# Performance work log

Measured on AMD Instinct MI355X. Metric: run time of the kernel, lower is better.

Reference implementation:

```python
import jax, jax.numpy as jnp
import numpy as np

BITS = 4
MAXQ = (1 << BITS) - 1          # 15
PACK = 32 // BITS               # 8 values per int32
IN_F = 4096
OUT_F = 11008


def setup_inputs() -> dict:
    key = jax.random.key(0)
    k1, k2, k3, k4, k5 = jax.random.split(key, 5)
    x = jax.random.normal(k1, (8, IN_F), dtype=jnp.float32)
    qweight = jax.random.randint(k2, (IN_F // 32 * BITS, OUT_F), 0, 2147483647, dtype=jnp.int32)
    qzeros = jax.random.randint(k3, (1, OUT_F // 32 * BITS), 0, 2147483647, dtype=jnp.int32)
    scales = jax.random.uniform(k4, (1, OUT_F), dtype=jnp.float32, minval=1e-3, maxval=2e-2)
    bias = jax.random.normal(k5, (OUT_F,), dtype=jnp.float32)
    return {"x": x, "qweight": qweight, "qzeros": qzeros, "scales": scales, "bias": bias}


def reference(x, qweight, qzeros, scales, bias):
    # GPTQ-style unpack: each int32 packs PACK values of BITS bits, LSB first.
    shifts = jnp.arange(0, 32, BITS, dtype=jnp.int32)  # wf
    # unpack weights: (IN_F//PACK, OUT_F) -> (IN_F//PACK, PACK, OUT_F) -> (IN_F, OUT_F)
    w = (qweight[:, None, :] >> shifts[None, :, None]) & MAXQ
    w = w.reshape(IN_F, OUT_F).astype(scales.dtype)
    # unpack zeros: (1, OUT_F//PACK) -> (1, OUT_F//PACK, PACK) -> (1, OUT_F), +1 per GPTQ convention
    z = ((qzeros[:, :, None] >> shifts[None, None, :]) & MAXQ) + 1
    z = z.reshape(1, OUT_F).astype(scales.dtype)
    # single quantization group (group_size == infeatures, g_idx all zeros)
    W = scales * (w - z)                      # (IN_F, OUT_F)
    return x @ W + bias
```

## Files before the change

kernel.cpp:

```cpp
#include <hip/hip_runtime.h>

#define IN_F 4096
#define OUT_F 11008
#define M 8
#define KROWS 512
#define KSLICES 16
#define ROWS_PER_SLICE (KROWS / KSLICES)

__global__ __launch_bounds__(256) void init_out_kernel(
    const float* __restrict__ bias, float* __restrict__ out)
{
    int idx = blockIdx.x * 256 + threadIdx.x;
    if (idx < M * OUT_F) {
        out[idx] = bias[idx % OUT_F];
    }
}

__global__ __launch_bounds__(256) void gptq_gemm_kernel(
    const float* __restrict__ x,
    const int*   __restrict__ qw,
    const int*   __restrict__ qz,
    const float* __restrict__ sc,
    float*       __restrict__ out)
{
    const int j = blockIdx.x * 256 + threadIdx.x;
    if (j >= OUT_F) return;
    const int i0 = blockIdx.y * ROWS_PER_SLICE;

    const int   zq = qz[j >> 3];
    const float zf = (float)(((zq >> ((j & 7) * 4)) & 15) + 1);
    const float s  = sc[j];

    float acc[M];
#pragma unroll
    for (int r = 0; r < M; ++r) acc[r] = 0.0f;

#pragma unroll 2
    for (int i = 0; i < ROWS_PER_SLICE; ++i) {
        const int q     = qw[(size_t)(i0 + i) * OUT_F + j];
        const int kbase = (i0 + i) * 8;
#pragma unroll
        for (int p = 0; p < 8; ++p) {
            const float wf = (float)((q >> (p * 4)) & 15) - zf;
#pragma unroll
            for (int r = 0; r < M; ++r) {
                acc[r] = fmaf(wf, x[r * IN_F + kbase + p], acc[r]);
            }
        }
    }

#pragma unroll
    for (int r = 0; r < M; ++r) {
        atomicAdd(&out[r * OUT_F + j], s * acc[r]);
    }
}

extern "C" void kernel_launch(void* const* d_in, const int* in_sizes, int n_in,
                              void* d_out, int out_size, void* d_ws, size_t ws_size,
                              hipStream_t stream) {
    const float* x    = (const float*)d_in[0];
    const int*   qw   = (const int*)d_in[1];
    const int*   qz   = (const int*)d_in[2];
    const float* sc   = (const float*)d_in[3];
    const float* bias = (const float*)d_in[4];
    float* out = (float*)d_out;

    int init_blocks = (M * OUT_F + 255) / 256;
    hipLaunchKernelGGL(init_out_kernel, dim3(init_blocks), dim3(256), 0, stream,
                       bias, out);

    dim3 grid(OUT_F / 256, KSLICES);
    hipLaunchKernelGGL(gptq_gemm_kernel, grid, dim3(256), 0, stream,
                       x, qw, qz, sc, out);
}
```

Measured before the change: 108.7 us.

## Replace atomic split-K with workspace partials, factored zero-point, and vectorized loads

```diff
diff --git a/kernel.cpp b/kernel.cpp
--- a/kernel.cpp
+++ b/kernel.cpp
@@ -4,55 +4,113 @@
 #define OUT_F 11008
 #define M 8
 #define KROWS 512
-#define KSLICES 16
-#define ROWS_PER_SLICE (KROWS / KSLICES)
+#define S_SLICES 32
+#define ROWS_PER_SLICE (KROWS / S_SLICES)
+#define GEMM_THREADS 128
+#define NJ4 (OUT_F / 4)
 
-__global__ __launch_bounds__(256) void init_out_kernel(
-    const float* __restrict__ bias, float* __restrict__ out)
+__global__ __launch_bounds__(64) void rowsum_kernel(
+    const float* __restrict__ x, float* __restrict__ rs)
 {
-    int idx = blockIdx.x * 256 + threadIdx.x;
-    if (idx < M * OUT_F) {
-        out[idx] = bias[idx % OUT_F];
+    const int r = blockIdx.x;
+    const int t = threadIdx.x;
+    const float4* xp = (const float4*)(x + (size_t)r * IN_F);
+    float s = 0.0f;
+#pragma unroll
+    for (int c = 0; c < 16; ++c) {
+        float4 v = xp[c * 64 + t];
+        s += v.x + v.y + v.z + v.w;
     }
+#pragma unroll
+    for (int off = 1; off < 64; off <<= 1) s += __shfl_xor(s, off, 64);
+    if (t == 0) rs[r] = s;
 }
 
-__global__ __launch_bounds__(256) void gptq_gemm_kernel(
+__global__ __launch_bounds__(GEMM_THREADS) void gptq_gemm_partial(
     const float* __restrict__ x,
     const int*   __restrict__ qw,
-    const int*   __restrict__ qz,
-    const float* __restrict__ sc,
-    float*       __restrict__ out)
+    float*       __restrict__ P)
 {
-    const int j = blockIdx.x * 256 + threadIdx.x;
-    if (j >= OUT_F) return;
+    const int t  = threadIdx.x;
+    const int j0 = blockIdx.x * (GEMM_THREADS * 2) + 2 * t;
     const int i0 = blockIdx.y * ROWS_PER_SLICE;
 
-    const int   zq = qz[j >> 3];
-    const float zf = (float)(((zq >> ((j & 7) * 4)) & 15) + 1);
-    const float s  = sc[j];
+    float acc[M][2];
+#pragma unroll
+    for (int r = 0; r < M; ++r) { acc[r][0] = 0.0f; acc[r][1] = 0.0f; }
 
-    float acc[M];
+    for (int i = 0; i < ROWS_PER_SLICE; ++i) {
+        const int row = i0 + i;
+        const int2 q = *(const int2*)(qw + (size_t)row * OUT_F + j0);
+        const int kb = row * 8;
+
+        float4 xa[M], xb[M];
 #pragma unroll
-    for (int r = 0; r < M; ++r) acc[r] = 0.0f;
+        for (int r = 0; r < M; ++r) {
+            const float* xp = x + (size_t)r * IN_F + kb;
+            xa[r] = *(const float4*)xp;
+            xb[r] = *(const float4*)(xp + 4);
+        }
 
-#pragma unroll 2
-    for (int i = 0; i < ROWS_PER_SLICE; ++i) {
-        const int q     = qw[(size_t)(i0 + i) * OUT_F + j];
-        const int kbase = (i0 + i) * 8;
 #pragma unroll
         for (int p = 0; p < 8; ++p) {
-            const float wf = (float)((q >> (p * 4)) & 15) - zf;
+            const float w0 = (float)((q.x >> (4 * p)) & 15);
+            const float w1 = (float)((q.y >> (4 * p)) & 15);
 #pragma unroll
             for (int r = 0; r < M; ++r) {
-                acc[r] = fmaf(wf, x[r * IN_F + kbase + p], acc[r]);
+                const float xv = (p < 4) ? ((const float*)&xa[r])[p]
+                                         : ((const float*)&xb[r])[p - 4];
+                acc[r][0] = fmaf(w0, xv, acc[r][0]);
+                acc[r][1] = fmaf(w1, xv, acc[r][1]);
             }
         }
     }
 
+    float* Pp = P + (size_t)blockIdx.y * M * OUT_F;
 #pragma unroll
     for (int r = 0; r < M; ++r) {
-        atomicAdd(&out[r * OUT_F + j], s * acc[r]);
+        float2 v; v.x = acc[r][0]; v.y = acc[r][1];
+        *(float2*)(Pp + (size_t)r * OUT_F + j0) = v;
     }
+}
+
+__global__ __launch_bounds__(256) void reduce_kernel(
+    const float* __restrict__ P,
+    const float* __restrict__ rs,
+    const int*   __restrict__ qz,
+    const float* __restrict__ sc,
+    const float* __restrict__ bias,
+    float*       __restrict__ out)
+{
+    const int idx = blockIdx.x * 256 + threadIdx.x;
+    const int jq  = idx % NJ4;
+    const int r   = idx / NJ4;
+    const int j0  = jq * 4;
+
+    float4 acc = {0.0f, 0.0f, 0.0f, 0.0f};
+#pragma unroll 8
+    for (int s = 0; s < S_SLICES; ++s) {
+        const float4 v = *(const float4*)(P + (size_t)s * M * OUT_F + (size_t)r * OUT_F + j0);
+        acc.x += v.x; acc.y += v.y; acc.z += v.z; acc.w += v.w;
+    }
+
+    const int zw = qz[j0 >> 3];
+    const int sh = (j0 & 7) * 4;
+    const float z0 = (float)(((zw >> (sh     )) & 15) + 1);
+    const float z1 = (float)(((zw >> (sh +  4)) & 15) + 1);
+    const float z2 = (float)(((zw >> (sh +  8)) & 15) + 1);
+    const float z3 = (float)(((zw >> (sh + 12)) & 15) + 1);
+
+    const float rsum = rs[r];
+    const float4 s4 = *(const float4*)(sc + j0);
+    const float4 b4 = *(const float4*)(bias + j0);
+
+    float4 o;
+    o.x = fmaf(s4.x, acc.x - z0 * rsum, b4.x);
+    o.y = fmaf(s4.y, acc.y - z1 * rsum, b4.y);
+    o.z = fmaf(s4.z, acc.z - z2 * rsum, b4.z);
+    o.w = fmaf(s4.w, acc.w - z3 * rsum, b4.w);
+    *(float4*)(out + (size_t)r * OUT_F + j0) = o;
 }
 
 extern "C" void kernel_launch(void* const* d_in, const int* in_sizes, int n_in,
@@ -65,11 +123,15 @@
     const float* bias = (const float*)d_in[4];
     float* out = (float*)d_out;
 
-    int init_blocks = (M * OUT_F + 255) / 256;
-    hipLaunchKernelGGL(init_out_kernel, dim3(init_blocks), dim3(256), 0, stream,
-                       bias, out);
+    float* P  = (float*)d_ws;
+    float* rs = P + (size_t)S_SLICES * M * OUT_F;
 
-    dim3 grid(OUT_F / 256, KSLICES);
-    hipLaunchKernelGGL(gptq_gemm_kernel, grid, dim3(256), 0, stream,
-                       x, qw, qz, sc, out);
+    hipLaunchKernelGGL(rowsum_kernel, dim3(M), dim3(64), 0, stream, x, rs);
+
+    dim3 grid(OUT_F / (GEMM_THREADS * 2), S_SLICES);
+    hipLaunchKernelGGL(gptq_gemm_partial, grid, dim3(GEMM_THREADS), 0, stream,
+                       x, qw, P);
+
+    hipLaunchKernelGGL(reduce_kernel, dim3((M * NJ4) / 256), dim3(256), 0, stream,
+                       P, rs, qz, sc, bias, out);
 }
```

After: 96.62 us. -11.1%, faster.
